# Performance work log

Hardware: AMD Instinct MI355X
Metric: run time of the kernel (lower is better)

Reference implementation:

```python
import jax, jax.numpy as jnp
import numpy as np

D = 64          # dim1 = dim2 = dim3
B = 512         # batch
MMHID = 256
F = (D + 1) ** 3  # 274625, encoder1 input size
SKIP = 3 * (D + 1)  # 195


def _lin(x, w, b):
    # torch nn.Linear: y = x @ W^T + b, W: [out, in]
    return x @ w.T + b


def _bilinear(x1, x2, w, b):
    # torch nn.Bilinear: y_o = x1_i W_{oij} x2_j + b_o
    return jnp.einsum('bi,oij,bj->bo', x1, w, x2) + b


def setup_inputs() -> dict:
    key = jax.random.key(0)
    ks = jax.random.split(key, 16)

    def n(k, shape, scale):
        return (jax.random.normal(k, shape, dtype=jnp.float32) * scale)

    inp = {
        'vec1': n(ks[0], (B, D), 1.0),
        'vec2': n(ks[1], (B, D), 1.0),
        'vec3': n(ks[2], (B, D), 1.0),
        # gated branch 1
        'h1_w': n(ks[3], (D, D), 1.0 / np.sqrt(D)), 'h1_b': jnp.zeros((D,), jnp.float32),
        'z1_w': n(ks[4], (D, D, D), 1.0 / D), 'z1_b': jnp.zeros((D,), jnp.float32),
        'o1_w': n(ks[5], (D, D), 1.0 / np.sqrt(D)), 'o1_b': jnp.zeros((D,), jnp.float32),
        # gated branch 2
        'h2_w': n(ks[6], (D, D), 1.0 / np.sqrt(D)), 'h2_b': jnp.zeros((D,), jnp.float32),
        'z2_w': n(ks[7], (D, D, D), 1.0 / D), 'z2_b': jnp.zeros((D,), jnp.float32),
        'o2_w': n(ks[8], (D, D), 1.0 / np.sqrt(D)), 'o2_b': jnp.zeros((D,), jnp.float32),
        # gated branch 3
        'h3_w': n(ks[9], (D, D), 1.0 / np.sqrt(D)), 'h3_b': jnp.zeros((D,), jnp.float32),
        'z3_w': n(ks[10], (D, D, D), 1.0 / D), 'z3_b': jnp.zeros((D,), jnp.float32),
        'o3_w': n(ks[11], (D, D), 1.0 / np.sqrt(D)), 'o3_b': jnp.zeros((D,), jnp.float32),
        # encoders
        'enc1_w': n(ks[12], (MMHID, F), 1.0 / np.sqrt(F)), 'enc1_b': jnp.zeros((MMHID,), jnp.float32),
        'enc2_w': n(ks[13], (MMHID, MMHID + SKIP), 1.0 / np.sqrt(MMHID + SKIP)), 'enc2_b': jnp.zeros((MMHID,), jnp.float32),
    }
    return inp


def reference(vec1, vec2, vec3,
              h1_w, h1_b, z1_w, z1_b, o1_w, o1_b,
              h2_w, h2_b, z2_w, z2_b, o2_w, o2_b,
              h3_w, h3_b, z3_w, z3_b, o3_w, o3_b,
              enc1_w, enc1_b, enc2_w, enc2_b):
    # dropout layers are identity in eval mode
    h1 = jax.nn.relu(_lin(vec1, h1_w, h1_b))
    z1 = _bilinear(vec1, vec3, z1_w, z1_b)
    o1 = jax.nn.relu(_lin(jax.nn.sigmoid(z1) * h1, o1_w, o1_b))

    h2 = jax.nn.relu(_lin(vec2, h2_w, h2_b))
    z2 = _bilinear(vec2, vec3, z2_w, z2_b)
    o2 = jax.nn.relu(_lin(jax.nn.sigmoid(z2) * h2, o2_w, o2_b))

    h3 = jax.nn.relu(_lin(vec3, h3_w, h3_b))
    z3 = _bilinear(vec1, vec3, z3_w, z3_b)  # note: z3 uses (vec1, vec3) per source
    o3 = jax.nn.relu(_lin(jax.nn.sigmoid(z3) * h3, o3_w, o3_b))

    ones = jnp.ones((o1.shape[0], 1), o1.dtype)
    o1 = jnp.concatenate([o1, ones], axis=1)  # [B, D+1]
    o2 = jnp.concatenate([o2, ones], axis=1)
    o3 = jnp.concatenate([o3, ones], axis=1)

    # trilinear outer product, flattened in (i, j, k) order matching
    # bmm(o1, o2).flatten then bmm(., o3).flatten in torch
    o123 = jnp.einsum('bi,bj,bk->bijk', o1, o2, o3).reshape(o1.shape[0], -1)  # [B, F]

    out = jax.nn.relu(_lin(o123, enc1_w, enc1_b))
    out = jnp.concatenate([out, o1, o2, o3], axis=1)  # skip connection
    out = jax.nn.relu(_lin(out, enc2_w, enc2_b))
    return out
```

## Files before the change

kernel.cpp:

```cpp
#include <hip/hip_runtime.h>
#include <hip/hip_bf16.h>
#include <stdint.h>

typedef unsigned short u16;
typedef unsigned int u32;

#define F1 274625
#define IJ1 4225

typedef float v4f __attribute__((ext_vector_type(4)));
typedef __bf16 v8bf __attribute__((ext_vector_type(8)));

__device__ __forceinline__ float lof(u32 u) { union { u32 u; float f; } c; c.u = u << 16; return c.f; }
__device__ __forceinline__ u16 f2bf(float f) {
  union { float f; u32 u; } c; c.f = f;
  u32 r = (c.u >> 16) & 1u;
  return (u16)((c.u + 0x7fffu + r) >> 16);
}
__device__ __forceinline__ u32 pkbf(u32 a, u32 b) {
  union { float f; u32 u; } ca, cb; ca.u = a; cb.u = b;
  __hip_bfloat162 h = __float22bfloat162_rn(make_float2(ca.f, cb.f));
  union { __hip_bfloat162 h; u32 u; } c; c.h = h; return c.u;
}

__global__ void __launch_bounds__(256) k0_transpose(const float* __restrict__ v1,
    const float* __restrict__ v2, const float* __restrict__ v3, float* __restrict__ xT) {
  int g = blockIdx.x * 256 + threadIdx.x;
  if (g >= 3 * 64 * 512) return;
  int t = g >> 15, r = g & 32767;
  int d = r >> 9, b = r & 511;
  const float* v = (t == 0) ? v1 : ((t == 1) ? v2 : v3);
  xT[g] = v[b * 64 + d];
}

__global__ void __launch_bounds__(256) k3t_w2t(const float* __restrict__ w2,
                                               float* __restrict__ w2T) {
  __shared__ float t[32][33];
  int bx = blockIdx.x & 7, by = blockIdx.x >> 3;
  int tx = threadIdx.x & 31, ty = threadIdx.x >> 5;
  int c = by * 32 + tx;
#pragma unroll
  for (int r = 0; r < 32; r += 8) {
    int o = bx * 32 + ty + r;
    t[ty + r][tx] = (c < 451) ? w2[o * 451 + c] : 0.f;
  }
  __syncthreads();
#pragma unroll
  for (int r = 0; r < 32; r += 8) {
    int cc = by * 32 + ty + r;
    if (cc < 451) w2T[cc * 256 + bx * 32 + tx] = t[tx][ty + r];
  }
}

__global__ void __launch_bounds__(256) k1_bilinear(
    const float* __restrict__ zw1, const float* __restrict__ zw2, const float* __restrict__ zw3,
    const float* __restrict__ xT, float* __restrict__ zsum) {
  int bid = blockIdx.x;
  int ih = bid & 1, bh = (bid >> 1) & 1;
  int o = (bid >> 2) & 63, t = bid >> 8;
  int b = bh * 256 + threadIdx.x;
  const float* zw = (t == 0) ? zw1 : ((t == 1) ? zw2 : zw3);
  const float* xiT = xT + ((t == 1) ? 32768 : 0);
  const float* x3T = xT + 65536;
  float x3r[64];
#pragma unroll
  for (int j = 0; j < 64; ++j) x3r[j] = x3T[j * 512 + b];
  const float4* w4 = (const float4*)(zw + o * 4096);
  float acc = 0.f;
  int i0 = ih * 32;
#pragma unroll 4
  for (int i = i0; i < i0 + 32; ++i) {
    float xi = xiT[i * 512 + b];
    float s = 0.f;
#pragma unroll
    for (int q = 0; q < 16; ++q) {
      float4 w = w4[i * 16 + q];
      s += w.x * x3r[q*4+0] + w.y * x3r[q*4+1] + w.z * x3r[q*4+2] + w.w * x3r[q*4+3];
    }
    acc += xi * s;
  }
  zsum[ih * 98304 + t * 32768 + o * 512 + b] = acc;
}

__global__ void __launch_bounds__(256) k2_branch(
    const float* __restrict__ hw1, const float* __restrict__ hb1,
    const float* __restrict__ ow1, const float* __restrict__ ob1,
    const float* __restrict__ hw2, const float* __restrict__ hb2,
    const float* __restrict__ ow2, const float* __restrict__ ob2,
    const float* __restrict__ hw3, const float* __restrict__ hb3,
    const float* __restrict__ ow3, const float* __restrict__ ob3,
    const float* __restrict__ zb1, const float* __restrict__ zb2, const float* __restrict__ zb3,
    const float* __restrict__ xT, const float* __restrict__ zsum,
    float* __restrict__ oT, u16* __restrict__ o3row) {
  int t = blockIdx.x >> 3, bc = blockIdx.x & 7;
  int lane = threadIdx.x & 63;
  int w = __builtin_amdgcn_readfirstlane((int)(threadIdx.x >> 6));
  int b = bc * 64 + lane;
  const float* hw = (t==0)?hw1:((t==1)?hw2:hw3);
  const float* hb = (t==0)?hb1:((t==1)?hb2:hb3);
  const float* ow = (t==0)?ow1:((t==1)?ow2:ow3);
  const float* ob = (t==0)?ob1:((t==1)?ob2:ob3);
  const float* zb = (t==0)?zb1:((t==1)?zb2:zb3);
  const float* xtT = xT + t * 32768;
  const float4* hw4 = (const float4*)hw;
  const float4* ow4 = (const float4*)ow;
  __shared__ float gT[64][68];
  float xr[64];
#pragma unroll
  for (int k = 0; k < 64; ++k) xr[k] = xtT[k * 512 + b];
#pragma unroll
  for (int ii = 0; ii < 16; ii += 4) {
    float gv[4];
#pragma unroll
    for (int q = 0; q < 4; ++q) {
      int i = w * 16 + ii + q;
      float a = hb[i];
#pragma unroll
      for (int kq = 0; kq < 16; ++kq) {
        float4 h4 = hw4[i * 16 + kq];
        a += h4.x * xr[kq*4+0] + h4.y * xr[kq*4+1] + h4.z * xr[kq*4+2] + h4.w * xr[kq*4+3];
      }
      float hv = fmaxf(a, 0.f);
      int zi = t * 32768 + i * 512 + b;
      float z = zsum[zi] + zsum[98304 + zi] + zb[i];
      float sg = 1.f / (1.f + __expf(-z));
      gv[q] = sg * hv;
    }
    *(float4*)&gT[lane][w * 16 + ii] = make_float4(gv[0], gv[1], gv[2], gv[3]);
  }
  __syncthreads();
  float gr[64];
#pragma unroll
  for (int k = 0; k < 64; k += 4) {
    float4 g4 = *(const float4*)&gT[lane][k];
    gr[k] = g4.x; gr[k+1] = g4.y; gr[k+2] = g4.z; gr[k+3] = g4.w;
  }
#pragma unroll
  for (int ii = 0; ii < 16; ++ii) {
    int oo = w * 16 + ii;
    float a = ob[oo];
#pragma unroll
    for (int kq = 0; kq < 16; ++kq) {
      float4 o4 = ow4[oo * 16 + kq];
      a += o4.x * gr[kq*4+0] + o4.y * gr[kq*4+1] + o4.z * gr[kq*4+2] + o4.w * gr[kq*4+3];
    }
    float ov = fmaxf(a, 0.f);
    oT[(t * 65 + oo) * 512 + b] = ov;
    if (t == 2) o3row[b * 72 + oo] = f2bf(ov);
  }
  if (w == 0) oT[(t * 65 + 64) * 512 + b] = 1.f;
  if (t == 2 && w == 1) {
    uint4 ones = make_uint4(0x3F80u, 0u, 0u, 0u);
    *(uint4*)&o3row[b * 72 + 64] = ones;
  }
}

template<int S4>
__device__ __forceinline__ void pack_row(const uint4* qv, u16* bp, u16* vvp,
                                         int row, int hh) {
  u32 l[36];
#pragma unroll
  for (int r = 0; r < 9; ++r) {
    l[4*r+0] = qv[r].x; l[4*r+1] = qv[r].y; l[4*r+2] = qv[r].z; l[4*r+3] = qv[r].w;
  }
  int rp = (row >> 2) + 2 * (row & 3);
#pragma unroll
  for (int cl = 0; cl < 4; ++cl) {
    u32 p0 = pkbf(l[S4+8*cl+0], l[S4+8*cl+1]);
    u32 p1 = pkbf(l[S4+8*cl+2], l[S4+8*cl+3]);
    u32 p2 = pkbf(l[S4+8*cl+4], l[S4+8*cl+5]);
    u32 p3 = pkbf(l[S4+8*cl+6], l[S4+8*cl+7]);
    int pos = (hh * 4 + cl + rp) & 7;
    *(uint4*)(bp + (pos << 3)) = make_uint4(p0, p1, p2, p3);
  }
  if (hh) vvp[row] = (u16)(pkbf(l[S4+32], l[S4+32]) & 0xffffu);
}

__global__ void __launch_bounds__(256, 2) k4_gemm(
    const float* __restrict__ W, const u16* __restrict__ o3row,
    const float* __restrict__ oT, float* __restrict__ accum,
    float* __restrict__ pbuf, int mode) {
  __shared__ u16 o3r[128 * 64];
  __shared__ u16 Bs[2][128 * 64];
  __shared__ u16 vvs[2][128];
  __shared__ float o12sf[2][128];
  int bid = blockIdx.x;
  int xcd = bid & 7, slot = bid >> 3;
  int mb = slot & 3, ph = slot >> 2;
  int pair = ph * 8 + xcd;
  int sK = pair >> 1, nb = pair & 1;
  int mbase = mb * 128, nbase = nb * 128;
  int ij0 = (sK * IJ1) >> 6, ij1 = ((sK + 1) * IJ1) >> 6;
  int tid = threadIdx.x;
  int lane = tid & 63;
  int wid = __builtin_amdgcn_readfirstlane(tid >> 6);
  int wm = wid >> 1, wn = wid & 1;
  int lrow = lane & 15, lkg = lane >> 4;
  int rpos = lane >> 1, hh = lane & 1;

  v4f acc[16] = {};
  const uint4* Wq = (const uint4*)W;
  uint4 qa[9], qb[9];
  float aA = 0.f, aB = 0.f, bA = 0.f, bB = 0.f;

  auto loadW = [&](int ij, uint4* q) {
    int cc = (wid - ij) & 3;
    int row = rpos * 4 + cc;
    long g = (long)(nbase + row) * F1 + (long)ij * 65;
    long u4 = (g >> 2) + (long)hh * 8;
#pragma unroll
    for (int r = 0; r < 9; ++r) q[r] = Wq[u4 + r];
  };
  auto loadO = [&](int ij, float& A, float& B) {
    if (tid < 128) {
      int i = ij / 65, j = ij - i * 65;
      A = oT[i * 512 + mbase + tid];
      B = oT[(65 + j) * 512 + mbase + tid];
    }
  };
  auto packCur = [&](int ij, int buf, const uint4* q, float pA, float pB) {
    int cc = (wid - ij) & 3;
    int row = rpos * 4 + cc;
    u16* bp = &Bs[buf][row << 6];
    if      (wid == 0) pack_row<0>(q, bp, &vvs[buf][0], row, hh);
    else if (wid == 1) pack_row<1>(q, bp, &vvs[buf][0], row, hh);
    else if (wid == 2) pack_row<2>(q, bp, &vvs[buf][0], row, hh);
    else               pack_row<3>(q, bp, &vvs[buf][0], row, hh);
    if (tid < 128) o12sf[buf][tid] = pA * pB;
  };

  loadW(ij0, qa); loadO(ij0, aA, aB);

  for (int u = tid; u < 1024; u += 256) {
    int r = u >> 3, c = u & 7;
    uint4 v = *(const uint4*)(o3row + (mbase + r) * 72 + c * 8);
    int pos = (c + (r >> 2) + 2 * (r & 3)) & 7;
    *(uint4*)&o3r[(r << 6) + (pos << 3)] = v;
  }

  loadW(ij0 + 1, qb); loadO(ij0 + 1, bA, bB);

  int aoff[4][2], boff[4][2], vvr[4];
#pragma unroll
  for (int u = 0; u < 4; ++u) {
    int ra = wm * 64 + u * 16 + lrow;
    int rb = wn * 64 + u * 16 + lrow;
#pragma unroll
    for (int k2 = 0; k2 < 2; ++k2) {
      aoff[u][k2] = (ra << 6) + (((k2 * 4 + lkg + (ra >> 2) + 2 * (ra & 3)) & 7) << 3);
      boff[u][k2] = (rb << 6) + (((k2 * 4 + lkg + (rb >> 2) + 2 * (rb & 3)) & 7) << 3);
    }
    vvr[u] = rb;
  }

  __syncthreads();
  packCur(ij0, 0, qa, aA, aB);
  loadW(ij0 + 2, qa); loadO(ij0 + 2, aA, aB);
  asm volatile("s_waitcnt lgkmcnt(0)\n\ts_barrier" ::: "memory");

#pragma unroll 1
  for (int ij = ij0; ij < ij1; ++ij) {
    int cur = (ij - ij0) & 1;
    if (ij + 1 < ij1) {
      if (cur == 0) {
        packCur(ij + 1, 1, qb, bA, bB);
        if (ij + 3 < ij1) { loadW(ij + 3, qb); loadO(ij + 3, bA, bB); }
      } else {
        packCur(ij + 1, 0, qa, aA, aB);
        if (ij + 3 < ij1) { loadW(ij + 3, qa); loadO(ij + 3, aA, aB); }
      }
    }
    const u16* bs = Bs[cur];
    v8bf bfr[4][2];
#pragma unroll
    for (int u2 = 0; u2 < 4; ++u2)
#pragma unroll
      for (int k2 = 0; k2 < 2; ++k2)
        bfr[u2][k2] = *(const v8bf*)&bs[boff[u2][k2]];
    float vv[4];
#pragma unroll
    for (int u2 = 0; u2 < 4; ++u2) vv[u2] = lof((u32)vvs[cur][vvr[u2]]);
    __builtin_amdgcn_s_setprio(1);
#pragma unroll
    for (int t2 = 0; t2 < 4; ++t2) {
      v8bf a0 = *(const v8bf*)&o3r[aoff[t2][0]];
      v8bf a1 = *(const v8bf*)&o3r[aoff[t2][1]];
      v4f P0 = {}, P1 = {}, P2 = {}, P3 = {};
      P0 = __builtin_amdgcn_mfma_f32_16x16x32_bf16(a0, bfr[0][0], P0, 0, 0, 0);
      P0 = __builtin_amdgcn_mfma_f32_16x16x32_bf16(a1, bfr[0][1], P0, 0, 0, 0);
      P1 = __builtin_amdgcn_mfma_f32_16x16x32_bf16(a0, bfr[1][0], P1, 0, 0, 0);
      P1 = __builtin_amdgcn_mfma_f32_16x16x32_bf16(a1, bfr[1][1], P1, 0, 0, 0);
      P2 = __builtin_amdgcn_mfma_f32_16x16x32_bf16(a0, bfr[2][0], P2, 0, 0, 0);
      P2 = __builtin_amdgcn_mfma_f32_16x16x32_bf16(a1, bfr[2][1], P2, 0, 0, 0);
      P3 = __builtin_amdgcn_mfma_f32_16x16x32_bf16(a0, bfr[3][0], P3, 0, 0, 0);
      P3 = __builtin_amdgcn_mfma_f32_16x16x32_bf16(a1, bfr[3][1], P3, 0, 0, 0);
      float4 sp = *(const float4*)&o12sf[cur][wm * 64 + t2 * 16 + lkg * 4];
#pragma unroll
      for (int e = 0; e < 4; ++e) {
        float se = (e == 0) ? sp.x : (e == 1) ? sp.y : (e == 2) ? sp.z : sp.w;
        acc[t2 * 4 + 0][e] += se * (P0[e] + vv[0]);
        acc[t2 * 4 + 1][e] += se * (P1[e] + vv[1]);
        acc[t2 * 4 + 2][e] += se * (P2[e] + vv[2]);
        acc[t2 * 4 + 3][e] += se * (P3[e] + vv[3]);
      }
    }
    __builtin_amdgcn_s_setprio(0);
    asm volatile("s_waitcnt lgkmcnt(0)\n\ts_barrier" ::: "memory");
  }

  if (mode) {
    float* dst = pbuf + ((long)sK << 17);
#pragma unroll
    for (int t2 = 0; t2 < 4; ++t2) {
      int gb0 = mbase + wm * 64 + t2 * 16 + lkg * 4;
#pragma unroll
      for (int u2 = 0; u2 < 4; ++u2) {
        int go = nbase + wn * 64 + u2 * 16 + lrow;
#pragma unroll
        for (int e = 0; e < 4; ++e)
          dst[(gb0 + e) * 256 + go] = acc[t2 * 4 + u2][e];
      }
    }
  } else {
#pragma unroll
    for (int t2 = 0; t2 < 4; ++t2) {
      int gb0 = mbase + wm * 64 + t2 * 16 + lkg * 4;
#pragma unroll
      for (int u2 = 0; u2 < 4; ++u2) {
        int go = nbase + wn * 64 + u2 * 16 + lrow;
#pragma unroll
        for (int e = 0; e < 4; ++e)
          atomicAdd(&accum[(gb0 + e) * 256 + go], acc[t2 * 4 + u2][e]);
      }
    }
  }
}

__global__ void __launch_bounds__(256) k4_reduce(const float* __restrict__ P,
    const float* __restrict__ e1b, float* __restrict__ xrT) {
  int g = blockIdx.x * 256 + threadIdx.x;
  const v4f* p4 = (const v4f*)P;
  v4f s = p4[g];
#pragma unroll 4
  for (int k = 1; k < 64; ++k) s += p4[(k << 15) + g];
  int b = g >> 6, c0 = (g & 63) << 2;
#pragma unroll
  for (int e = 0; e < 4; ++e)
    xrT[(c0 + e) * 512 + b] = fmaxf(s[e] + e1b[c0 + e], 0.f);
}

__global__ void __launch_bounds__(256) k5v_enc2(const float* __restrict__ xrT,
    const float* __restrict__ oT, const float* __restrict__ w2T,
    const float* __restrict__ enc2b, float* __restrict__ outp) {
  __shared__ float xl[451 * 8 + 8];
  int b0 = blockIdx.x * 8;
  int tid = threadIdx.x;
  for (int u = tid; u < 3608; u += 256) {
    int c = u >> 3, bi = u & 7;
    xl[u] = (c < 256) ? xrT[c * 512 + b0 + bi] : oT[(c - 256) * 512 + b0 + bi];
  }
  float a[8];
  float bv = enc2b[tid];
#pragma unroll
  for (int q = 0; q < 8; ++q) a[q] = bv;
  __syncthreads();
#pragma unroll 4
  for (int c = 0; c < 451; ++c) {
    float w = w2T[c * 256 + tid];
    float4 x0 = *(const float4*)&xl[c * 8];
    float4 x1 = *(const float4*)&xl[c * 8 + 4];
    a[0] += w * x0.x; a[1] += w * x0.y; a[2] += w * x0.z; a[3] += w * x0.w;
    a[4] += w * x1.x; a[5] += w * x1.y; a[6] += w * x1.z; a[7] += w * x1.w;
  }
#pragma unroll
  for (int q = 0; q < 8; ++q) outp[(b0 + q) * 256 + tid] = fmaxf(a[q], 0.f);
}

__global__ void __launch_bounds__(256) k5_enc2(
    const float* __restrict__ xin, const float* __restrict__ oT,
    const float* __restrict__ enc1b, const float* __restrict__ w2,
    const float* __restrict__ enc2b, float* __restrict__ outp) {
  int bg = blockIdx.x >> 3, og = blockIdx.x & 7;
  int lane = threadIdx.x & 63;
  int w = __builtin_amdgcn_readfirstlane((int)(threadIdx.x >> 6));
  int b = bg * 64 + lane;
  int obase = og * 32 + w * 8;
  float a8[8];
#pragma unroll
  for (int q = 0; q < 8; ++q) a8[q] = enc2b[obase + q];
  for (int c = 0; c < 256; ++c) {
    float x = fmaxf(xin[b * 256 + c] + enc1b[c], 0.f);
#pragma unroll
    for (int q = 0; q < 8; ++q) a8[q] += w2[(obase + q) * 451 + c] * x;
  }
  for (int e = 0; e < 195; ++e) {
    float x = oT[e * 512 + b];
#pragma unroll
    for (int q = 0; q < 8; ++q) a8[q] += w2[(obase + q) * 451 + 256 + e] * x;
  }
#pragma unroll
  for (int q = 0; q < 8; ++q) outp[b * 256 + obase + q] = fmaxf(a8[q], 0.f);
}

extern "C" void kernel_launch(void* const* d_in, const int* in_sizes, int n_in,
                              void* d_out, int out_size, void* d_ws, size_t ws_size,
                              hipStream_t stream) {
  const float* vec1 = (const float*)d_in[0];
  const float* vec2 = (const float*)d_in[1];
  const float* vec3 = (const float*)d_in[2];
  const float* h1w = (const float*)d_in[3];  const float* h1b = (const float*)d_in[4];
  const float* z1w = (const float*)d_in[5];  const float* z1b = (const float*)d_in[6];
  const float* o1w = (const float*)d_in[7];  const float* o1b = (const float*)d_in[8];
  const float* h2w = (const float*)d_in[9];  const float* h2b = (const float*)d_in[10];
  const float* z2w = (const float*)d_in[11]; const float* z2b = (const float*)d_in[12];
  const float* o2w = (const float*)d_in[13]; const float* o2b = (const float*)d_in[14];
  const float* h3w = (const float*)d_in[15]; const float* h3b = (const float*)d_in[16];
  const float* z3w = (const float*)d_in[17]; const float* z3b = (const float*)d_in[18];
  const float* o3w = (const float*)d_in[19]; const float* o3b = (const float*)d_in[20];
  const float* e1w = (const float*)d_in[21]; const float* e1b = (const float*)d_in[22];
  const float* e2w = (const float*)d_in[23]; const float* e2b = (const float*)d_in[24];

  char* ws = (char*)d_ws;
  float* accum = (float*)(ws + 0);
  float* oT    = (float*)(ws + 524288);
  u16* o3row   = (u16*)  (ws + 923648);
  float* xT    = (float*)(ws + 997376);
  float* zsum  = (float*)(ws + 1390592);
  float* w2T   = (float*)(ws + 2177024);
  float* pbuf  = (float*)(ws + 2638848);
  size_t need = 2638848 + (size_t)64 * 512 * 256 * 4;
  int mode = (ws_size >= need) ? 1 : 0;
  float* pArg = mode ? pbuf : accum;

  if (!mode) hipMemsetAsync(accum, 0, 524288, stream);

  hipLaunchKernelGGL(k0_transpose, dim3(384), dim3(256), 0, stream, vec1, vec2, vec3, xT);
  if (mode)
    hipLaunchKernelGGL(k3t_w2t, dim3(120), dim3(256), 0, stream, e2w, w2T);
  hipLaunchKernelGGL(k1_bilinear, dim3(768), dim3(256), 0, stream,
                     z1w, z2w, z3w, xT, zsum);
  hipLaunchKernelGGL(k2_branch, dim3(24), dim3(256), 0, stream,
                     h1w, h1b, o1w, o1b, h2w, h2b, o2w, o2b, h3w, h3b, o3w, o3b,
                     z1b, z2b, z3b, xT, zsum, oT, o3row);
  hipLaunchKernelGGL(k4_gemm, dim3(512), dim3(256), 0, stream, e1w, o3row, oT, accum,
                     pArg, mode);
  if (mode) {
    hipLaunchKernelGGL(k4_reduce, dim3(128), dim3(256), 0, stream, pbuf, e1b, accum);
    hipLaunchKernelGGL(k5v_enc2, dim3(64), dim3(256), 0, stream, accum, oT, w2T, e2b,
                       (float*)d_out);
  } else {
    hipLaunchKernelGGL(k5_enc2, dim3(64), dim3(256), 0, stream, accum, oT, e1b, e2w, e2b,
                       (float*)d_out);
  }
}
```

Baseline: 738.4 us.

## Retile enc1 GEMM to 64-row M tiles with 48 K-splits and stage small weights in LDS

The main enc1 GEMM now uses 64-batch M tiles with A fragments (o3 rows) held in registers rather than LDS. The K dimension is split 48 ways instead of 64, and the launch grows to 768 blocks with 3 blocks per CU. The bilinear kernel stops splitting i and stages each 64x64 weight slice in LDS, and the branch kernel stages its h/o weights and biases in LDS. Together these aim to cut LDS traffic and improve occupancy and balance for the weight-streaming GEMM, at the cost of re-reading the enc1 weights once per M tile (8 times instead of 4) and more per-thread work in the bilinear kernel.

```diff
diff --git a/kernel.cpp b/kernel.cpp
--- a/kernel.cpp
+++ b/kernel.cpp
@@ -7,6 +7,7 @@
 
 #define F1 274625
 #define IJ1 4225
+#define NSK 48
 
 typedef float v4f __attribute__((ext_vector_type(4)));
 typedef __bf16 v8bf __attribute__((ext_vector_type(8)));
@@ -55,31 +56,38 @@
 __global__ void __launch_bounds__(256) k1_bilinear(
     const float* __restrict__ zw1, const float* __restrict__ zw2, const float* __restrict__ zw3,
     const float* __restrict__ xT, float* __restrict__ zsum) {
+  __shared__ float wsm[4096];
   int bid = blockIdx.x;
-  int ih = bid & 1, bh = (bid >> 1) & 1;
-  int o = (bid >> 2) & 63, t = bid >> 8;
-  int b = bh * 256 + threadIdx.x;
+  int bh = bid & 1, o = (bid >> 1) & 63, t = bid >> 7;
+  int tid = threadIdx.x;
   const float* zw = (t == 0) ? zw1 : ((t == 1) ? zw2 : zw3);
+  {
+    const float4* src = (const float4*)(zw + o * 4096);
+    float4* dst = (float4*)wsm;
+#pragma unroll
+    for (int u = 0; u < 4; ++u) dst[u * 256 + tid] = src[u * 256 + tid];
+  }
+  int b = bh * 256 + tid;
   const float* xiT = xT + ((t == 1) ? 32768 : 0);
   const float* x3T = xT + 65536;
   float x3r[64];
 #pragma unroll
   for (int j = 0; j < 64; ++j) x3r[j] = x3T[j * 512 + b];
-  const float4* w4 = (const float4*)(zw + o * 4096);
+  __syncthreads();
   float acc = 0.f;
-  int i0 = ih * 32;
-#pragma unroll 4
-  for (int i = i0; i < i0 + 32; ++i) {
+#pragma unroll 2
+  for (int i = 0; i < 64; ++i) {
     float xi = xiT[i * 512 + b];
     float s = 0.f;
+    const float4* w4 = (const float4*)&wsm[i * 64];
 #pragma unroll
     for (int q = 0; q < 16; ++q) {
-      float4 w = w4[i * 16 + q];
+      float4 w = w4[q];
       s += w.x * x3r[q*4+0] + w.y * x3r[q*4+1] + w.z * x3r[q*4+2] + w.w * x3r[q*4+3];
     }
     acc += xi * s;
   }
-  zsum[ih * 98304 + t * 32768 + o * 512 + b] = acc;
+  zsum[t * 32768 + o * 512 + b] = acc;
 }
 
 __global__ void __launch_bounds__(256) k2_branch(
@@ -92,37 +100,50 @@
     const float* __restrict__ zb1, const float* __restrict__ zb2, const float* __restrict__ zb3,
     const float* __restrict__ xT, const float* __restrict__ zsum,
     float* __restrict__ oT, u16* __restrict__ o3row) {
+  __shared__ float hws[4096];
+  __shared__ float ows[4096];
+  __shared__ float hbs[64], obs[64], zbs[64];
+  __shared__ float gT[64][68];
   int t = blockIdx.x >> 3, bc = blockIdx.x & 7;
-  int lane = threadIdx.x & 63;
-  int w = __builtin_amdgcn_readfirstlane((int)(threadIdx.x >> 6));
+  int tid = threadIdx.x;
+  int lane = tid & 63;
+  int w = __builtin_amdgcn_readfirstlane((int)(tid >> 6));
   int b = bc * 64 + lane;
   const float* hw = (t==0)?hw1:((t==1)?hw2:hw3);
   const float* hb = (t==0)?hb1:((t==1)?hb2:hb3);
   const float* ow = (t==0)?ow1:((t==1)?ow2:ow3);
   const float* ob = (t==0)?ob1:((t==1)?ob2:ob3);
   const float* zb = (t==0)?zb1:((t==1)?zb2:zb3);
+  {
+    const float4* hs = (const float4*)hw;
+    const float4* os = (const float4*)ow;
+    float4* hd = (float4*)hws;
+    float4* od = (float4*)ows;
+#pragma unroll
+    for (int u = 0; u < 4; ++u) { hd[u * 256 + tid] = hs[u * 256 + tid];
+                                  od[u * 256 + tid] = os[u * 256 + tid]; }
+    if (tid < 64) { hbs[tid] = hb[tid]; obs[tid] = ob[tid]; zbs[tid] = zb[tid]; }
+  }
   const float* xtT = xT + t * 32768;
-  const float4* hw4 = (const float4*)hw;
-  const float4* ow4 = (const float4*)ow;
-  __shared__ float gT[64][68];
   float xr[64];
 #pragma unroll
   for (int k = 0; k < 64; ++k) xr[k] = xtT[k * 512 + b];
+  __syncthreads();
 #pragma unroll
   for (int ii = 0; ii < 16; ii += 4) {
     float gv[4];
 #pragma unroll
     for (int q = 0; q < 4; ++q) {
       int i = w * 16 + ii + q;
-      float a = hb[i];
+      float a = hbs[i];
+      const float4* h4 = (const float4*)&hws[i * 64];
 #pragma unroll
       for (int kq = 0; kq < 16; ++kq) {
-        float4 h4 = hw4[i * 16 + kq];
-        a += h4.x * xr[kq*4+0] + h4.y * xr[kq*4+1] + h4.z * xr[kq*4+2] + h4.w * xr[kq*4+3];
+        float4 h = h4[kq];
+        a += h.x * xr[kq*4+0] + h.y * xr[kq*4+1] + h.z * xr[kq*4+2] + h.w * xr[kq*4+3];
       }
       float hv = fmaxf(a, 0.f);
-      int zi = t * 32768 + i * 512 + b;
-      float z = zsum[zi] + zsum[98304 + zi] + zb[i];
+      float z = zsum[t * 32768 + i * 512 + b] + zbs[i];
       float sg = 1.f / (1.f + __expf(-z));
       gv[q] = sg * hv;
     }
@@ -138,11 +159,12 @@
 #pragma unroll
   for (int ii = 0; ii < 16; ++ii) {
     int oo = w * 16 + ii;
-    float a = ob[oo];
+    float a = obs[oo];
+    const float4* o4 = (const float4*)&ows[oo * 64];
 #pragma unroll
     for (int kq = 0; kq < 16; ++kq) {
-      float4 o4 = ow4[oo * 16 + kq];
-      a += o4.x * gr[kq*4+0] + o4.y * gr[kq*4+1] + o4.z * gr[kq*4+2] + o4.w * gr[kq*4+3];
+      float4 o = o4[kq];
+      a += o.x * gr[kq*4+0] + o.y * gr[kq*4+1] + o.z * gr[kq*4+2] + o.w * gr[kq*4+3];
     }
     float ov = fmaxf(a, 0.f);
     oT[(t * 65 + oo) * 512 + b] = ov;
@@ -176,29 +198,27 @@
   if (hh) vvp[row] = (u16)(pkbf(l[S4+32], l[S4+32]) & 0xffffu);
 }
 
-__global__ void __launch_bounds__(256, 2) k4_gemm(
+__global__ void __launch_bounds__(256, 3) k4_gemm(
     const float* __restrict__ W, const u16* __restrict__ o3row,
     const float* __restrict__ oT, float* __restrict__ accum,
     float* __restrict__ pbuf, int mode) {
-  __shared__ u16 o3r[128 * 64];
   __shared__ u16 Bs[2][128 * 64];
   __shared__ u16 vvs[2][128];
-  __shared__ float o12sf[2][128];
+  __shared__ float o12sf[2][64];
   int bid = blockIdx.x;
   int xcd = bid & 7, slot = bid >> 3;
-  int mb = slot & 3, ph = slot >> 2;
+  int mb = slot & 7, ph = slot >> 3;
   int pair = ph * 8 + xcd;
   int sK = pair >> 1, nb = pair & 1;
-  int mbase = mb * 128, nbase = nb * 128;
-  int ij0 = (sK * IJ1) >> 6, ij1 = ((sK + 1) * IJ1) >> 6;
+  int mbase = mb * 64, nbase = nb * 128;
+  int ij0 = (sK * IJ1) / NSK, ij1 = ((sK + 1) * IJ1) / NSK;
   int tid = threadIdx.x;
   int lane = tid & 63;
   int wid = __builtin_amdgcn_readfirstlane(tid >> 6);
-  int wm = wid >> 1, wn = wid & 1;
   int lrow = lane & 15, lkg = lane >> 4;
   int rpos = lane >> 1, hh = lane & 1;
 
-  v4f acc[16] = {};
+  v4f acc[8] = {};
   const uint4* Wq = (const uint4*)W;
   uint4 qa[9], qb[9];
   float aA = 0.f, aB = 0.f, bA = 0.f, bB = 0.f;
@@ -212,7 +232,7 @@
     for (int r = 0; r < 9; ++r) q[r] = Wq[u4 + r];
   };
   auto loadO = [&](int ij, float& A, float& B) {
-    if (tid < 128) {
+    if (tid < 64) {
       int i = ij / 65, j = ij - i * 65;
       A = oT[i * 512 + mbase + tid];
       B = oT[(65 + j) * 512 + mbase + tid];
@@ -226,34 +246,29 @@
     else if (wid == 1) pack_row<1>(q, bp, &vvs[buf][0], row, hh);
     else if (wid == 2) pack_row<2>(q, bp, &vvs[buf][0], row, hh);
     else               pack_row<3>(q, bp, &vvs[buf][0], row, hh);
-    if (tid < 128) o12sf[buf][tid] = pA * pB;
+    if (tid < 64) o12sf[buf][tid] = pA * pB;
   };
 
   loadW(ij0, qa); loadO(ij0, aA, aB);
-
-  for (int u = tid; u < 1024; u += 256) {
-    int r = u >> 3, c = u & 7;
-    uint4 v = *(const uint4*)(o3row + (mbase + r) * 72 + c * 8);
-    int pos = (c + (r >> 2) + 2 * (r & 3)) & 7;
-    *(uint4*)&o3r[(r << 6) + (pos << 3)] = v;
-  }
-
   loadW(ij0 + 1, qb); loadO(ij0 + 1, bA, bB);
 
-  int aoff[4][2], boff[4][2], vvr[4];
-#pragma unroll
-  for (int u = 0; u < 4; ++u) {
-    int ra = wm * 64 + u * 16 + lrow;
-    int rb = wn * 64 + u * 16 + lrow;
-#pragma unroll
-    for (int k2 = 0; k2 < 2; ++k2) {
-      aoff[u][k2] = (ra << 6) + (((k2 * 4 + lkg + (ra >> 2) + 2 * (ra & 3)) & 7) << 3);
-      boff[u][k2] = (rb << 6) + (((k2 * 4 + lkg + (rb >> 2) + 2 * (rb & 3)) & 7) << 3);
-    }
-    vvr[u] = rb;
-  }
-
-  __syncthreads();
+  v8bf af[4][2];
+#pragma unroll
+  for (int t2 = 0; t2 < 4; ++t2)
+#pragma unroll
+    for (int k2 = 0; k2 < 2; ++k2)
+      af[t2][k2] = *(const v8bf*)&o3row[(mbase + t2 * 16 + lrow) * 72 + k2 * 32 + lkg * 8];
+
+  int boff[2][2], vvr[2];
+#pragma unroll
+  for (int u2 = 0; u2 < 2; ++u2) {
+    int rb = wid * 32 + u2 * 16 + lrow;
+#pragma unroll
+    for (int k2 = 0; k2 < 2; ++k2)
+      boff[u2][k2] = (rb << 6) + (((k2 * 4 + lkg + (rb >> 2) + 2 * (rb & 3)) & 7) << 3);
+    vvr[u2] = rb;
+  }
+
   packCur(ij0, 0, qa, aA, aB);
   loadW(ij0 + 2, qa); loadO(ij0 + 2, aA, aB);
   asm volatile("s_waitcnt lgkmcnt(0)\n\ts_barrier" ::: "memory");
@@ -271,37 +286,28 @@
       }
     }
     const u16* bs = Bs[cur];
-    v8bf bfr[4][2];
-#pragma unroll
-    for (int u2 = 0; u2 < 4; ++u2)
-#pragma unroll
-      for (int k2 = 0; k2 < 2; ++k2)
-        bfr[u2][k2] = *(const v8bf*)&bs[boff[u2][k2]];
-    float vv[4];
-#pragma unroll
-    for (int u2 = 0; u2 < 4; ++u2) vv[u2] = lof((u32)vvs[cur][vvr[u2]]);
+    v8bf bf0[2], bf1[2];
+#pragma unroll
+    for (int k2 = 0; k2 < 2; ++k2) {
+      bf0[k2] = *(const v8bf*)&bs[boff[0][k2]];
+      bf1[k2] = *(const v8bf*)&bs[boff[1][k2]];
+    }
+    float vv0 = lof((u32)vvs[cur][vvr[0]]);
+    float vv1 = lof((u32)vvs[cur][vvr[1]]);
     __builtin_amdgcn_s_setprio(1);
 #pragma unroll
     for (int t2 = 0; t2 < 4; ++t2) {
-      v8bf a0 = *(const v8bf*)&o3r[aoff[t2][0]];
-      v8bf a1 = *(const v8bf*)&o3r[aoff[t2][1]];
-      v4f P0 = {}, P1 = {}, P2 = {}, P3 = {};
-      P0 = __builtin_amdgcn_mfma_f32_16x16x32_bf16(a0, bfr[0][0], P0, 0, 0, 0);
-      P0 = __builtin_amdgcn_mfma_f32_16x16x32_bf16(a1, bfr[0][1], P0, 0, 0, 0);
-      P1 = __builtin_amdgcn_mfma_f32_16x16x32_bf16(a0, bfr[1][0], P1, 0, 0, 0);
-      P1 = __builtin_amdgcn_mfma_f32_16x16x32_bf16(a1, bfr[1][1], P1, 0, 0, 0);
-      P2 = __builtin_amdgcn_mfma_f32_16x16x32_bf16(a0, bfr[2][0], P2, 0, 0, 0);
-      P2 = __builtin_amdgcn_mfma_f32_16x16x32_bf16(a1, bfr[2][1], P2, 0, 0, 0);
-      P3 = __builtin_amdgcn_mfma_f32_16x16x32_bf16(a0, bfr[3][0], P3, 0, 0, 0);
-      P3 = __builtin_amdgcn_mfma_f32_16x16x32_bf16(a1, bfr[3][1], P3, 0, 0, 0);
-      float4 sp = *(const float4*)&o12sf[cur][wm * 64 + t2 * 16 + lkg * 4];
+      v4f P0 = {}, P1 = {};
+      P0 = __builtin_amdgcn_mfma_f32_16x16x32_bf16(af[t2][0], bf0[0], P0, 0, 0, 0);
+      P0 = __builtin_amdgcn_mfma_f32_16x16x32_bf16(af[t2][1], bf0[1], P0, 0, 0, 0);
+      P1 = __builtin_amdgcn_mfma_f32_16x16x32_bf16(af[t2][0], bf1[0], P1, 0, 0, 0);
+      P1 = __builtin_amdgcn_mfma_f32_16x16x32_bf16(af[t2][1], bf1[1], P1, 0, 0, 0);
+      float4 sp = *(const float4*)&o12sf[cur][t2 * 16 + lkg * 4];
 #pragma unroll
       for (int e = 0; e < 4; ++e) {
         float se = (e == 0) ? sp.x : (e == 1) ? sp.y : (e == 2) ? sp.z : sp.w;
-        acc[t2 * 4 + 0][e] += se * (P0[e] + vv[0]);
-        acc[t2 * 4 + 1][e] += se * (P1[e] + vv[1]);
-        acc[t2 * 4 + 2][e] += se * (P2[e] + vv[2]);
-        acc[t2 * 4 + 3][e] += se * (P3[e] + vv[3]);
+        acc[t2 * 2 + 0][e] += se * (P0[e] + vv0);
+        acc[t2 * 2 + 1][e] += se * (P1[e] + vv1);
       }
     }
     __builtin_amdgcn_s_setprio(0);
@@ -312,25 +318,25 @@
     float* dst = pbuf + ((long)sK << 17);
 #pragma unroll
     for (int t2 = 0; t2 < 4; ++t2) {
-      int gb0 = mbase + wm * 64 + t2 * 16 + lkg * 4;
-#pragma unroll
-      for (int u2 = 0; u2 < 4; ++u2) {
-        int go = nbase + wn * 64 + u2 * 16 + lrow;
+      int gb0 = mbase + t2 * 16 + lkg * 4;
+#pragma unroll
+      for (int u2 = 0; u2 < 2; ++u2) {
+        int go = nbase + wid * 32 + u2 * 16 + lrow;
 #pragma unroll
         for (int e = 0; e < 4; ++e)
-          dst[(gb0 + e) * 256 + go] = acc[t2 * 4 + u2][e];
+          dst[(gb0 + e) * 256 + go] = acc[t2 * 2 + u2][e];
       }
     }
   } else {
 #pragma unroll
     for (int t2 = 0; t2 < 4; ++t2) {
-      int gb0 = mbase + wm * 64 + t2 * 16 + lkg * 4;
-#pragma unroll
-      for (int u2 = 0; u2 < 4; ++u2) {
-        int go = nbase + wn * 64 + u2 * 16 + lrow;
+      int gb0 = mbase + t2 * 16 + lkg * 4;
+#pragma unroll
+      for (int u2 = 0; u2 < 2; ++u2) {
+        int go = nbase + wid * 32 + u2 * 16 + lrow;
 #pragma unroll
         for (int e = 0; e < 4; ++e)
-          atomicAdd(&accum[(gb0 + e) * 256 + go], acc[t2 * 4 + u2][e]);
+          atomicAdd(&accum[(gb0 + e) * 256 + go], acc[t2 * 2 + u2][e]);
       }
     }
   }
@@ -342,7 +348,7 @@
   const v4f* p4 = (const v4f*)P;
   v4f s = p4[g];
 #pragma unroll 4
-  for (int k = 1; k < 64; ++k) s += p4[(k << 15) + g];
+  for (int k = 1; k < NSK; ++k) s += p4[(k << 15) + g];
   int b = g >> 6, c0 = (g & 63) << 2;
 #pragma unroll
   for (int e = 0; e < 4; ++e)
@@ -426,9 +432,9 @@
   u16* o3row   = (u16*)  (ws + 923648);
   float* xT    = (float*)(ws + 997376);
   float* zsum  = (float*)(ws + 1390592);
-  float* w2T   = (float*)(ws + 2177024);
-  float* pbuf  = (float*)(ws + 2638848);
-  size_t need = 2638848 + (size_t)64 * 512 * 256 * 4;
+  float* w2T   = (float*)(ws + 1783808);
+  float* pbuf  = (float*)(ws + 2245632);
+  size_t need = 2245632 + (size_t)NSK * 512 * 256 * 4;
   int mode = (ws_size >= need) ? 1 : 0;
   float* pArg = mode ? pbuf : accum;
 
@@ -437,12 +443,12 @@
   hipLaunchKernelGGL(k0_transpose, dim3(384), dim3(256), 0, stream, vec1, vec2, vec3, xT);
   if (mode)
     hipLaunchKernelGGL(k3t_w2t, dim3(120), dim3(256), 0, stream, e2w, w2T);
-  hipLaunchKernelGGL(k1_bilinear, dim3(768), dim3(256), 0, stream,
+  hipLaunchKernelGGL(k1_bilinear, dim3(384), dim3(256), 0, stream,
                      z1w, z2w, z3w, xT, zsum);
   hipLaunchKernelGGL(k2_branch, dim3(24), dim3(256), 0, stream,
                      h1w, h1b, o1w, o1b, h2w, h2b, o2w, o2b, h3w, h3b, o3w, o3b,
                      z1b, z2b, z3b, xT, zsum, oT, o3row);
-  hipLaunchKernelGGL(k4_gemm, dim3(512), dim3(256), 0, stream, e1w, o3row, oT, accum,
+  hipLaunchKernelGGL(k4_gemm, dim3(768), dim3(256), 0, stream, e1w, o3row, oT, accum,
                      pArg, mode);
   if (mode) {
     hipLaunchKernelGGL(k4_reduce, dim3(128), dim3(256), 0, stream, pbuf, e1b, accum);
```

New measurement: 1.087 ms. +47.2%, slower.
